# Performance work log

Hardware: AMD Instinct MI355X
Metric: run time of the kernel (lower is better)

The kernel has to match this reference:

```python
import jax, jax.numpy as jnp
import numpy as np

EMBED_DIM = 1024
NUM_HEADS = 16
HEAD_DIM = EMBED_DIM // NUM_HEADS
BATCH = 8
SEQ = 1024


def setup_inputs() -> dict:
    key = jax.random.key(0)
    ks = jax.random.split(key, 10)
    s = 1.0 / np.sqrt(EMBED_DIM)
    x = jax.random.normal(ks[0], (BATCH, SEQ, EMBED_DIM), dtype=jnp.float32)
    mask = jax.random.randint(ks[1], (BATCH, SEQ), 0, 2, dtype=jnp.int32)
    mk = lambda k: (jax.random.normal(k, (EMBED_DIM, EMBED_DIM), dtype=jnp.float32) * s)
    return {
        "x": x, "mask": mask,
        "Wq": mk(ks[2]), "bq": jnp.zeros((EMBED_DIM,), jnp.float32),
        "Wk": mk(ks[3]), "bk": jnp.zeros((EMBED_DIM,), jnp.float32),
        "Wv": mk(ks[4]), "bv": jnp.zeros((EMBED_DIM,), jnp.float32),
        "Wo": mk(ks[5]), "bo": jnp.zeros((EMBED_DIM,), jnp.float32),
    }


def _split_heads(t):
    # (B, S, E) -> (B, H, S, D)
    B, S, _ = t.shape
    return t.reshape(B, S, NUM_HEADS, HEAD_DIM).transpose(0, 2, 1, 3)


def reference(x, mask, Wq, bq, Wk, bk, Wv, bv, Wo, bo):
    B, S, E = x.shape
    # torch Linear: y = x @ W.T + b, weight shape (out, in)
    Q = _split_heads(jnp.einsum('bse,oe->bso', x, Wq) + bq)
    K = _split_heads(jnp.einsum('bse,oe->bso', x, Wk) + bk)
    V = _split_heads(jnp.einsum('bse,oe->bso', x, Wv) + bv)
    scores = jnp.einsum('bhqd,bhkd->bhqk', Q, K) / np.sqrt(HEAD_DIM)
    scores = jnp.clip(scores, -50.0, 50.0)
    m = (mask == 0)[:, None, None, :]  # (B,1,1,S)
    scores = jnp.where(m, jnp.float32(-1e9), scores)
    scores = jnp.where(jnp.isfinite(scores), scores, jnp.zeros_like(scores))
    aw = jax.nn.softmax(scores, axis=-1)
    aw = jnp.where(jnp.isfinite(aw), aw, jnp.zeros_like(aw))
    aw = aw / (aw.sum(axis=-1, keepdims=True) + 1e-10)
    # dropout is identity in eval mode
    attended = jnp.einsum('bhqk,bhkd->bhqd', aw, V)
    attended = attended.transpose(0, 2, 1, 3).reshape(B, S, E)
    output = jnp.einsum('bse,oe->bso', attended, Wo) + bo
    return (output, aw)
```

## Files before the change

### kernel.cpp

```cpp
#include <hip/hip_runtime.h>

typedef _Float16 f16x8 __attribute__((ext_vector_type(8)));
typedef float    f32x4 __attribute__((ext_vector_type(4)));

#define SEQL 1024
#define EMB  1024
#define NH   16
#define HD   64
#define BATCH 8

__global__ __launch_bounds__(256) void k_cvt_f32_f16(const float* __restrict__ in,
                                                     _Float16* __restrict__ out,
                                                     int n8) {
  int i = blockIdx.x * 256 + threadIdx.x;
  if (i >= n8) return;
  const float4* p = (const float4*)in;
  float4 a = p[2 * i], b = p[2 * i + 1];
  f16x8 o;
  o[0] = (_Float16)a.x; o[1] = (_Float16)a.y; o[2] = (_Float16)a.z; o[3] = (_Float16)a.w;
  o[4] = (_Float16)b.x; o[5] = (_Float16)b.y; o[6] = (_Float16)b.z; o[7] = (_Float16)b.w;
  ((f16x8*)out)[i] = o;
}

template <int OUT_F16>
__global__ __launch_bounds__(256) void k_gemm_nt(const _Float16* __restrict__ A,
                                                 const _Float16* __restrict__ B,
                                                 const float* __restrict__ bias,
                                                 void* __restrict__ Cv,
                                                 int M, int N, int K) {
  __shared__ __align__(16) _Float16 As[128 * 32];
  __shared__ __align__(16) _Float16 Bs[128 * 32];
  const int nb = N >> 7;
  const int bm = (int)blockIdx.x / nb, bn = (int)blockIdx.x % nb;
  const int m0 = bm << 7, n0 = bn << 7;
  const int tid = threadIdx.x;
  const int wave = tid >> 6, lane = tid & 63, quad = lane >> 4, l16 = lane & 15;
  const int wm = (wave & 1) << 6, wn = (wave >> 1) << 6;

  f32x4 acc[4][4] = {};

  const int c0 = tid, c1 = tid + 256;
  const int row0 = c0 >> 2, ko0 = (c0 & 3) << 3;
  const int row1 = c1 >> 2, ko1 = (c1 & 3) << 3;

  for (int k0 = 0; k0 < K; k0 += 32) {
    __syncthreads();
    ((uint4*)As)[c0] = *(const uint4*)(A + (size_t)(m0 + row0) * K + k0 + ko0);
    ((uint4*)As)[c1] = *(const uint4*)(A + (size_t)(m0 + row1) * K + k0 + ko1);
    ((uint4*)Bs)[c0] = *(const uint4*)(B + (size_t)(n0 + row0) * K + k0 + ko0);
    ((uint4*)Bs)[c1] = *(const uint4*)(B + (size_t)(n0 + row1) * K + k0 + ko1);
    __syncthreads();

    f16x8 af[4], bf[4];
#pragma unroll
    for (int i = 0; i < 4; ++i)
      af[i] = *(const f16x8*)(As + ((wm + (i << 4) + l16) << 5) + (quad << 3));
#pragma unroll
    for (int i = 0; i < 4; ++i)
      bf[i] = *(const f16x8*)(Bs + ((wn + (i << 4) + l16) << 5) + (quad << 3));
#pragma unroll
    for (int i = 0; i < 4; ++i)
#pragma unroll
      for (int j = 0; j < 4; ++j)
        acc[i][j] = __builtin_amdgcn_mfma_f32_16x16x32_f16(af[i], bf[j], acc[i][j], 0, 0, 0);
  }

#pragma unroll
  for (int j = 0; j < 4; ++j) {
    int col = n0 + wn + (j << 4) + l16;
    float bb = bias[col];
#pragma unroll
    for (int i = 0; i < 4; ++i) {
      int rowb = m0 + wm + (i << 4) + (quad << 2);
#pragma unroll
      for (int r = 0; r < 4; ++r) {
        float v = acc[i][j][r] + bb;
        if (OUT_F16)
          ((_Float16*)Cv)[(size_t)(rowb + r) * N + col] = (_Float16)v;
        else
          ((float*)Cv)[(size_t)(rowb + r) * N + col] = v;
      }
    }
  }
}

__global__ __launch_bounds__(256) void k_transpose_v(const _Float16* __restrict__ V,
                                                     _Float16* __restrict__ Vt) {
  int tid = blockIdx.x * 256 + threadIdx.x;
  int d = tid & 63;
  int s0 = ((tid >> 6) & 127) << 3;
  int h = (tid >> 13) & 15;
  int b = tid >> 17;
  const _Float16* src = V + ((size_t)(b * SEQL + s0)) * EMB + h * HD + d;
  f16x8 t;
#pragma unroll
  for (int j = 0; j < 8; ++j) t[j] = src[(size_t)j * EMB];
  *(f16x8*)(Vt + ((size_t)((b * NH + h) * HD + d)) * SEQL + s0) = t;
}

__global__ __launch_bounds__(256) void k_scores_softmax(const _Float16* __restrict__ Q,
                                                        const _Float16* __restrict__ Kmat,
                                                        const int* __restrict__ mask,
                                                        float* __restrict__ aw) {
  const int qt = blockIdx.x, h = blockIdx.y, b = blockIdx.z;
  const int tid = threadIdx.x;
  const int wave = tid >> 6, lane = tid & 63, quad = lane >> 4, l16 = lane & 15;

  const _Float16* Qbase = Q + ((size_t)(b * SEQL + qt * 16 + l16)) * EMB + h * HD + quad * 8;
  f16x8 qf0 = *(const f16x8*)(Qbase);
  f16x8 qf1 = *(const f16x8*)(Qbase + 32);

  float p[16][4];
  float mr[4], lr[4];
#pragma unroll
  for (int r = 0; r < 4; ++r) mr[r] = -3.0e38f;

  const int* mrow = mask + b * SEQL;

#pragma unroll
  for (int ct = 0; ct < 16; ++ct) {
    int col = wave * 256 + ct * 16 + l16;
    const _Float16* Kb = Kmat + ((size_t)(b * SEQL + col)) * EMB + h * HD + quad * 8;
    f16x8 kf0 = *(const f16x8*)(Kb);
    f16x8 kf1 = *(const f16x8*)(Kb + 32);
    f32x4 acc = {};
    acc = __builtin_amdgcn_mfma_f32_16x16x32_f16(qf0, kf0, acc, 0, 0, 0);
    acc = __builtin_amdgcn_mfma_f32_16x16x32_f16(qf1, kf1, acc, 0, 0, 0);
    bool mk = (mrow[col] == 0);
#pragma unroll
    for (int r = 0; r < 4; ++r) {
      float s = acc[r] * 0.125f;
      s = fminf(fmaxf(s, -50.f), 50.f);
      if (mk) s = -1.0e9f;
      p[ct][r] = s;
      mr[r] = fmaxf(mr[r], s);
    }
  }

#pragma unroll
  for (int r = 0; r < 4; ++r) {
    float m = mr[r];
    m = fmaxf(m, __shfl_xor(m, 1, 16));
    m = fmaxf(m, __shfl_xor(m, 2, 16));
    m = fmaxf(m, __shfl_xor(m, 4, 16));
    m = fmaxf(m, __shfl_xor(m, 8, 16));
    mr[r] = m;
  }

#pragma unroll
  for (int r = 0; r < 4; ++r) lr[r] = 0.f;
#pragma unroll
  for (int ct = 0; ct < 16; ++ct) {
#pragma unroll
    for (int r = 0; r < 4; ++r) {
      float e = __expf(p[ct][r] - mr[r]);
      p[ct][r] = e;
      lr[r] += e;
    }
  }
#pragma unroll
  for (int r = 0; r < 4; ++r) {
    float l = lr[r];
    l += __shfl_xor(l, 1, 16);
    l += __shfl_xor(l, 2, 16);
    l += __shfl_xor(l, 4, 16);
    l += __shfl_xor(l, 8, 16);
    lr[r] = l;
  }

  __shared__ float sm[4][16], sl[4][16];
  if (l16 == 0) {
#pragma unroll
    for (int r = 0; r < 4; ++r) {
      sm[wave][quad * 4 + r] = mr[r];
      sl[wave][quad * 4 + r] = lr[r];
    }
  }
  __syncthreads();

  float f[4];
#pragma unroll
  for (int r = 0; r < 4; ++r) {
    int row = quad * 4 + r;
    float M = fmaxf(fmaxf(sm[0][row], sm[1][row]), fmaxf(sm[2][row], sm[3][row]));
    float L = sl[0][row] * __expf(sm[0][row] - M) + sl[1][row] * __expf(sm[1][row] - M) +
              sl[2][row] * __expf(sm[2][row] - M) + sl[3][row] * __expf(sm[3][row] - M);
    f[r] = __expf(mr[r] - M) / L;
  }

  float* awb = aw + (((size_t)(b * NH + h)) * SEQL + qt * 16) * SEQL;
#pragma unroll
  for (int ct = 0; ct < 16; ++ct) {
    int col = wave * 256 + ct * 16 + l16;
#pragma unroll
    for (int r = 0; r < 4; ++r) {
      awb[(size_t)(quad * 4 + r) * SEQL + col] = p[ct][r] * f[r];
    }
  }
}

__global__ __launch_bounds__(256) void k_attn_pv(const float* __restrict__ aw,
                                                 const _Float16* __restrict__ Vt,
                                                 _Float16* __restrict__ att) {
  const int mt = blockIdx.x;
  const int h = blockIdx.y, b = blockIdx.z;
  const int tid = threadIdx.x;
  const int wave = tid >> 6, lane = tid & 63, quad = lane >> 4, l16 = lane & 15;
  const int m0 = mt * 64 + wave * 16;

  const float* awrow = aw + (((size_t)(b * NH + h)) * SEQL + m0 + l16) * SEQL;
  const _Float16* vtb = Vt + ((size_t)(b * NH + h)) * HD * SEQL;

  f32x4 acc[4] = {};

  for (int k0 = 0; k0 < SEQL; k0 += 32) {
    float4 a0 = *(const float4*)(awrow + k0 + quad * 8);
    float4 a1 = *(const float4*)(awrow + k0 + quad * 8 + 4);
    f16x8 af;
    af[0] = (_Float16)a0.x; af[1] = (_Float16)a0.y; af[2] = (_Float16)a0.z; af[3] = (_Float16)a0.w;
    af[4] = (_Float16)a1.x; af[5] = (_Float16)a1.y; af[6] = (_Float16)a1.z; af[7] = (_Float16)a1.w;
#pragma unroll
    for (int nt = 0; nt < 4; ++nt) {
      f16x8 bf = *(const f16x8*)(vtb + (size_t)(nt * 16 + l16) * SEQL + k0 + quad * 8);
      acc[nt] = __builtin_amdgcn_mfma_f32_16x16x32_f16(af, bf, acc[nt], 0, 0, 0);
    }
  }

#pragma unroll
  for (int nt = 0; nt < 4; ++nt) {
    int d = nt * 16 + l16;
#pragma unroll
    for (int r = 0; r < 4; ++r) {
      int srow = m0 + quad * 4 + r;
      att[((size_t)(b * SEQL + srow)) * EMB + h * HD + d] = (_Float16)acc[nt][r];
    }
  }
}

extern "C" void kernel_launch(void* const* d_in, const int* in_sizes, int n_in,
                              void* d_out, int out_size, void* d_ws, size_t ws_size,
                              hipStream_t stream) {
  const float* x  = (const float*)d_in[0];
  const int* mask = (const int*)d_in[1];
  const float* Wq = (const float*)d_in[2];
  const float* bq = (const float*)d_in[3];
  const float* Wk = (const float*)d_in[4];
  const float* bk = (const float*)d_in[5];
  const float* Wv = (const float*)d_in[6];
  const float* bv = (const float*)d_in[7];
  const float* Wo = (const float*)d_in[8];
  const float* bo = (const float*)d_in[9];

  float* out = (float*)d_out;
  float* aw = out + (size_t)BATCH * SEQL * EMB;

  char* ws = (char*)d_ws;
  _Float16* x16  = (_Float16*)(ws);
  _Float16* Wq16 = (_Float16*)(ws + ((size_t)16 << 20));
  _Float16* Wk16 = (_Float16*)(ws + ((size_t)18 << 20));
  _Float16* Wv16 = (_Float16*)(ws + ((size_t)20 << 20));
  _Float16* Wo16 = (_Float16*)(ws + ((size_t)22 << 20));
  _Float16* Q16  = (_Float16*)(ws + ((size_t)24 << 20));
  _Float16* K16  = (_Float16*)(ws + ((size_t)40 << 20));
  _Float16* V16  = (_Float16*)(ws + ((size_t)56 << 20));
  _Float16* Vt16  = x16;
  _Float16* att16 = Q16;

  const int M = BATCH * SEQL, N = EMB, K = EMB;

  k_cvt_f32_f16<<<4096, 256, 0, stream>>>(x, x16, (M * EMB) / 8);
  k_cvt_f32_f16<<<512, 256, 0, stream>>>(Wq, Wq16, (EMB * EMB) / 8);
  k_cvt_f32_f16<<<512, 256, 0, stream>>>(Wk, Wk16, (EMB * EMB) / 8);
  k_cvt_f32_f16<<<512, 256, 0, stream>>>(Wv, Wv16, (EMB * EMB) / 8);
  k_cvt_f32_f16<<<512, 256, 0, stream>>>(Wo, Wo16, (EMB * EMB) / 8);

  k_gemm_nt<1><<<(M / 128) * (N / 128), 256, 0, stream>>>(x16, Wq16, bq, Q16, M, N, K);
  k_gemm_nt<1><<<(M / 128) * (N / 128), 256, 0, stream>>>(x16, Wk16, bk, K16, M, N, K);
  k_gemm_nt<1><<<(M / 128) * (N / 128), 256, 0, stream>>>(x16, Wv16, bv, V16, M, N, K);

  k_transpose_v<<<4096, 256, 0, stream>>>(V16, Vt16);

  k_scores_softmax<<<dim3(SEQL / 16, NH, BATCH), 256, 0, stream>>>(Q16, K16, mask, aw);

  k_attn_pv<<<dim3(SEQL / 64, NH, BATCH), 256, 0, stream>>>(aw, Vt16, att16);

  k_gemm_nt<0><<<(M / 128) * (N / 128), 256, 0, stream>>>(att16, Wo16, bo, out, M, N, K);
}
```

Before: 1.044 ms.

## Fuse QKV GEMMs, merge conversions, fuse softmax with PV, use direct-to-LDS loads

```diff
diff --git a/kernel.cpp b/kernel.cpp
--- a/kernel.cpp
+++ b/kernel.cpp
@@ -1,4 +1,5 @@
 #include <hip/hip_runtime.h>
+#include <stdint.h>
 
 typedef _Float16 f16x8 __attribute__((ext_vector_type(8)));
 typedef float    f32x4 __attribute__((ext_vector_type(4)));
@@ -8,18 +9,52 @@
 #define NH   16
 #define HD   64
 #define BATCH 8
-
-__global__ __launch_bounds__(256) void k_cvt_f32_f16(const float* __restrict__ in,
-                                                     _Float16* __restrict__ out,
-                                                     int n8) {
-  int i = blockIdx.x * 256 + threadIdx.x;
-  if (i >= n8) return;
+#define QKVN 3072
+
+__device__ __forceinline__ void gll16(const void* g, void* l) {
+  __builtin_amdgcn_global_load_lds(
+      (const __attribute__((address_space(1))) unsigned int*)(uintptr_t)g,
+      (__attribute__((address_space(3))) unsigned int*)(uintptr_t)l, 16, 0, 0);
+}
+
+__device__ __forceinline__ void cvt8(const float* __restrict__ in,
+                                     _Float16* __restrict__ out, int i) {
   const float4* p = (const float4*)in;
   float4 a = p[2 * i], b = p[2 * i + 1];
   f16x8 o;
   o[0] = (_Float16)a.x; o[1] = (_Float16)a.y; o[2] = (_Float16)a.z; o[3] = (_Float16)a.w;
   o[4] = (_Float16)b.x; o[5] = (_Float16)b.y; o[6] = (_Float16)b.z; o[7] = (_Float16)b.w;
   ((f16x8*)out)[i] = o;
+}
+
+__global__ __launch_bounds__(256) void k_prep(const float* __restrict__ x,
+                                              const float* __restrict__ Wq,
+                                              const float* __restrict__ Wk,
+                                              const float* __restrict__ Wv,
+                                              const float* __restrict__ Wo,
+                                              const float* __restrict__ bq,
+                                              const float* __restrict__ bk,
+                                              const float* __restrict__ bv,
+                                              _Float16* __restrict__ x16,
+                                              _Float16* __restrict__ Wqkv16,
+                                              _Float16* __restrict__ Wo16,
+                                              float* __restrict__ bqkv) {
+  const int bid = blockIdx.x, tid = threadIdx.x;
+  if (bid < 4096) {
+    cvt8(x, x16, bid * 256 + tid);
+  } else if (bid < 4608) {
+    cvt8(Wq, Wqkv16, (bid - 4096) * 256 + tid);
+  } else if (bid < 5120) {
+    cvt8(Wk, Wqkv16 + (size_t)EMB * EMB, (bid - 4608) * 256 + tid);
+  } else if (bid < 5632) {
+    cvt8(Wv, Wqkv16 + (size_t)2 * EMB * EMB, (bid - 5120) * 256 + tid);
+  } else if (bid < 6144) {
+    cvt8(Wo, Wo16, (bid - 5632) * 256 + tid);
+  } else {
+    int i = (bid - 6144) * 256 + tid;
+    float v = (i < 1024) ? bq[i] : (i < 2048 ? bk[i - 1024] : bv[i - 2048]);
+    bqkv[i] = v;
+  }
 }
 
 template <int OUT_F16>
@@ -42,13 +77,17 @@
   const int c0 = tid, c1 = tid + 256;
   const int row0 = c0 >> 2, ko0 = (c0 & 3) << 3;
   const int row1 = c1 >> 2, ko1 = (c1 & 3) << 3;
+  const _Float16* a0 = A + (size_t)(m0 + row0) * K + ko0;
+  const _Float16* a1 = A + (size_t)(m0 + row1) * K + ko1;
+  const _Float16* b0 = B + (size_t)(n0 + row0) * K + ko0;
+  const _Float16* b1 = B + (size_t)(n0 + row1) * K + ko1;
 
   for (int k0 = 0; k0 < K; k0 += 32) {
     __syncthreads();
-    ((uint4*)As)[c0] = *(const uint4*)(A + (size_t)(m0 + row0) * K + k0 + ko0);
-    ((uint4*)As)[c1] = *(const uint4*)(A + (size_t)(m0 + row1) * K + k0 + ko1);
-    ((uint4*)Bs)[c0] = *(const uint4*)(B + (size_t)(n0 + row0) * K + k0 + ko0);
-    ((uint4*)Bs)[c1] = *(const uint4*)(B + (size_t)(n0 + row1) * K + k0 + ko1);
+    gll16(a0 + k0, As + (size_t)c0 * 8);
+    gll16(a1 + k0, As + (size_t)c1 * 8);
+    gll16(b0 + k0, Bs + (size_t)c0 * 8);
+    gll16(b1 + k0, Bs + (size_t)c1 * 8);
     __syncthreads();
 
     f16x8 af[4], bf[4];
@@ -84,29 +123,38 @@
   }
 }
 
-__global__ __launch_bounds__(256) void k_transpose_v(const _Float16* __restrict__ V,
+__global__ __launch_bounds__(256) void k_transpose_v(const _Float16* __restrict__ QKV,
                                                      _Float16* __restrict__ Vt) {
   int tid = blockIdx.x * 256 + threadIdx.x;
   int d = tid & 63;
   int s0 = ((tid >> 6) & 127) << 3;
   int h = (tid >> 13) & 15;
   int b = tid >> 17;
-  const _Float16* src = V + ((size_t)(b * SEQL + s0)) * EMB + h * HD + d;
+  const _Float16* src = QKV + ((size_t)(b * SEQL + s0)) * QKVN + 2048 + h * HD + d;
   f16x8 t;
 #pragma unroll
-  for (int j = 0; j < 8; ++j) t[j] = src[(size_t)j * EMB];
+  for (int j = 0; j < 8; ++j) t[j] = src[(size_t)j * QKVN];
   *(f16x8*)(Vt + ((size_t)((b * NH + h) * HD + d)) * SEQL + s0) = t;
 }
 
-__global__ __launch_bounds__(256) void k_scores_softmax(const _Float16* __restrict__ Q,
-                                                        const _Float16* __restrict__ Kmat,
-                                                        const int* __restrict__ mask,
-                                                        float* __restrict__ aw) {
+#define PPAD 272
+#define OPAD 68
+
+__global__ __launch_bounds__(256) void k_attn_fused(const _Float16* __restrict__ QKV,
+                                                    const _Float16* __restrict__ Vt,
+                                                    const int* __restrict__ mask,
+                                                    float* __restrict__ aw,
+                                                    _Float16* __restrict__ att) {
+  __shared__ __align__(16) _Float16 pbuf[4][16 * PPAD];
+  __shared__ float obuf[4][16 * OPAD];
+  __shared__ float sm[4][16], sl[4][16];
+
   const int qt = blockIdx.x, h = blockIdx.y, b = blockIdx.z;
   const int tid = threadIdx.x;
   const int wave = tid >> 6, lane = tid & 63, quad = lane >> 4, l16 = lane & 15;
 
-  const _Float16* Qbase = Q + ((size_t)(b * SEQL + qt * 16 + l16)) * EMB + h * HD + quad * 8;
+  const _Float16* Qbase =
+      QKV + ((size_t)(b * SEQL + qt * 16 + l16)) * QKVN + h * HD + quad * 8;
   f16x8 qf0 = *(const f16x8*)(Qbase);
   f16x8 qf1 = *(const f16x8*)(Qbase + 32);
 
@@ -116,11 +164,12 @@
   for (int r = 0; r < 4; ++r) mr[r] = -3.0e38f;
 
   const int* mrow = mask + b * SEQL;
+  const _Float16* Kb0 = QKV + (size_t)b * SEQL * QKVN + 1024 + h * HD + quad * 8;
 
 #pragma unroll
   for (int ct = 0; ct < 16; ++ct) {
     int col = wave * 256 + ct * 16 + l16;
-    const _Float16* Kb = Kmat + ((size_t)(b * SEQL + col)) * EMB + h * HD + quad * 8;
+    const _Float16* Kb = Kb0 + (size_t)col * QKVN;
     f16x8 kf0 = *(const f16x8*)(Kb);
     f16x8 kf1 = *(const f16x8*)(Kb + 32);
     f32x4 acc = {};
@@ -146,7 +195,6 @@
     m = fmaxf(m, __shfl_xor(m, 8, 16));
     mr[r] = m;
   }
-
 #pragma unroll
   for (int r = 0; r < 4; ++r) lr[r] = 0.f;
 #pragma unroll
@@ -167,8 +215,6 @@
     l += __shfl_xor(l, 8, 16);
     lr[r] = l;
   }
-
-  __shared__ float sm[4][16], sl[4][16];
   if (l16 == 0) {
 #pragma unroll
     for (int r = 0; r < 4; ++r) {
@@ -189,50 +235,46 @@
   }
 
   float* awb = aw + (((size_t)(b * NH + h)) * SEQL + qt * 16) * SEQL;
+  _Float16* pw = pbuf[wave];
 #pragma unroll
   for (int ct = 0; ct < 16; ++ct) {
-    int col = wave * 256 + ct * 16 + l16;
 #pragma unroll
     for (int r = 0; r < 4; ++r) {
-      awb[(size_t)(quad * 4 + r) * SEQL + col] = p[ct][r] * f[r];
-    }
-  }
-}
-
-__global__ __launch_bounds__(256) void k_attn_pv(const float* __restrict__ aw,
-                                                 const _Float16* __restrict__ Vt,
-                                                 _Float16* __restrict__ att) {
-  const int mt = blockIdx.x;
-  const int h = blockIdx.y, b = blockIdx.z;
-  const int tid = threadIdx.x;
-  const int wave = tid >> 6, lane = tid & 63, quad = lane >> 4, l16 = lane & 15;
-  const int m0 = mt * 64 + wave * 16;
-
-  const float* awrow = aw + (((size_t)(b * NH + h)) * SEQL + m0 + l16) * SEQL;
-  const _Float16* vtb = Vt + ((size_t)(b * NH + h)) * HD * SEQL;
-
-  f32x4 acc[4] = {};
-
-  for (int k0 = 0; k0 < SEQL; k0 += 32) {
-    float4 a0 = *(const float4*)(awrow + k0 + quad * 8);
-    float4 a1 = *(const float4*)(awrow + k0 + quad * 8 + 4);
-    f16x8 af;
-    af[0] = (_Float16)a0.x; af[1] = (_Float16)a0.y; af[2] = (_Float16)a0.z; af[3] = (_Float16)a0.w;
-    af[4] = (_Float16)a1.x; af[5] = (_Float16)a1.y; af[6] = (_Float16)a1.z; af[7] = (_Float16)a1.w;
+      float v = p[ct][r] * f[r];
+      awb[(size_t)(quad * 4 + r) * SEQL + wave * 256 + ct * 16 + l16] = v;
+      pw[(quad * 4 + r) * PPAD + ct * 16 + l16] = (_Float16)v;
+    }
+  }
+
+  f32x4 opv[4] = {};
+  const _Float16* vtb =
+      Vt + ((size_t)(b * NH + h)) * HD * SEQL + wave * 256 + quad * 8;
+#pragma unroll
+  for (int k = 0; k < 256; k += 32) {
+    f16x8 af = *(const f16x8*)(pw + l16 * PPAD + k + quad * 8);
 #pragma unroll
     for (int nt = 0; nt < 4; ++nt) {
-      f16x8 bf = *(const f16x8*)(vtb + (size_t)(nt * 16 + l16) * SEQL + k0 + quad * 8);
-      acc[nt] = __builtin_amdgcn_mfma_f32_16x16x32_f16(af, bf, acc[nt], 0, 0, 0);
-    }
-  }
-
-#pragma unroll
-  for (int nt = 0; nt < 4; ++nt) {
-    int d = nt * 16 + l16;
-#pragma unroll
-    for (int r = 0; r < 4; ++r) {
-      int srow = m0 + quad * 4 + r;
-      att[((size_t)(b * SEQL + srow)) * EMB + h * HD + d] = (_Float16)acc[nt][r];
+      f16x8 bf = *(const f16x8*)(vtb + (size_t)(nt * 16 + l16) * SEQL + k);
+      opv[nt] = __builtin_amdgcn_mfma_f32_16x16x32_f16(af, bf, opv[nt], 0, 0, 0);
+    }
+  }
+
+#pragma unroll
+  for (int nt = 0; nt < 4; ++nt)
+#pragma unroll
+    for (int r = 0; r < 4; ++r)
+      obuf[wave][(quad * 4 + r) * OPAD + nt * 16 + l16] = opv[nt][r];
+  __syncthreads();
+
+  {
+    int col = tid & 63;
+    int r0 = tid >> 6;
+#pragma unroll
+    for (int i = 0; i < 4; ++i) {
+      int row = r0 + i * 4;
+      float o = obuf[0][row * OPAD + col] + obuf[1][row * OPAD + col] +
+                obuf[2][row * OPAD + col] + obuf[3][row * OPAD + col];
+      att[((size_t)(b * SEQL + qt * 16 + row)) * EMB + h * HD + col] = (_Float16)o;
     }
   }
 }
@@ -255,34 +297,26 @@
   float* aw = out + (size_t)BATCH * SEQL * EMB;
 
   char* ws = (char*)d_ws;
-  _Float16* x16  = (_Float16*)(ws);
-  _Float16* Wq16 = (_Float16*)(ws + ((size_t)16 << 20));
-  _Float16* Wk16 = (_Float16*)(ws + ((size_t)18 << 20));
-  _Float16* Wv16 = (_Float16*)(ws + ((size_t)20 << 20));
-  _Float16* Wo16 = (_Float16*)(ws + ((size_t)22 << 20));
-  _Float16* Q16  = (_Float16*)(ws + ((size_t)24 << 20));
-  _Float16* K16  = (_Float16*)(ws + ((size_t)40 << 20));
-  _Float16* V16  = (_Float16*)(ws + ((size_t)56 << 20));
-  _Float16* Vt16  = x16;
-  _Float16* att16 = Q16;
-
-  const int M = BATCH * SEQL, N = EMB, K = EMB;
-
-  k_cvt_f32_f16<<<4096, 256, 0, stream>>>(x, x16, (M * EMB) / 8);
-  k_cvt_f32_f16<<<512, 256, 0, stream>>>(Wq, Wq16, (EMB * EMB) / 8);
-  k_cvt_f32_f16<<<512, 256, 0, stream>>>(Wk, Wk16, (EMB * EMB) / 8);
-  k_cvt_f32_f16<<<512, 256, 0, stream>>>(Wv, Wv16, (EMB * EMB) / 8);
-  k_cvt_f32_f16<<<512, 256, 0, stream>>>(Wo, Wo16, (EMB * EMB) / 8);
-
-  k_gemm_nt<1><<<(M / 128) * (N / 128), 256, 0, stream>>>(x16, Wq16, bq, Q16, M, N, K);
-  k_gemm_nt<1><<<(M / 128) * (N / 128), 256, 0, stream>>>(x16, Wk16, bk, K16, M, N, K);
-  k_gemm_nt<1><<<(M / 128) * (N / 128), 256, 0, stream>>>(x16, Wv16, bv, V16, M, N, K);
-
-  k_transpose_v<<<4096, 256, 0, stream>>>(V16, Vt16);
-
-  k_scores_softmax<<<dim3(SEQL / 16, NH, BATCH), 256, 0, stream>>>(Q16, K16, mask, aw);
-
-  k_attn_pv<<<dim3(SEQL / 64, NH, BATCH), 256, 0, stream>>>(aw, Vt16, att16);
-
-  k_gemm_nt<0><<<(M / 128) * (N / 128), 256, 0, stream>>>(att16, Wo16, bo, out, M, N, K);
-}
+  _Float16* x16    = (_Float16*)(ws);
+  _Float16* Wqkv16 = (_Float16*)(ws + ((size_t)16 << 20));
+  _Float16* Wo16   = (_Float16*)(ws + ((size_t)22 << 20));
+  float*    bqkv   = (float*)   (ws + ((size_t)24 << 20));
+  _Float16* QKV16  = (_Float16*)(ws + ((size_t)25 << 20));
+  _Float16* Vt16   = (_Float16*)(ws + ((size_t)73 << 20));
+  _Float16* att16  = (_Float16*)(ws + ((size_t)89 << 20));
+
+  const int M = BATCH * SEQL;
+
+  k_prep<<<6156, 256, 0, stream>>>(x, Wq, Wk, Wv, Wo, bq, bk, bv,
+                                   x16, Wqkv16, Wo16, bqkv);
+
+  k_gemm_nt<1><<<(M / 128) * (QKVN / 128), 256, 0, stream>>>(x16, Wqkv16, bqkv, QKV16,
+                                                             M, QKVN, EMB);
+
+  k_transpose_v<<<4096, 256, 0, stream>>>(QKV16, Vt16);
+
+  k_attn_fused<<<dim3(SEQL / 16, NH, BATCH), 256, 0, stream>>>(QKV16, Vt16, mask, aw, att16);
+
+  k_gemm_nt<0><<<(M / 128) * (EMB / 128), 256, 0, stream>>>(att16, Wo16, bo, out,
+                                                            M, EMB, EMB);
+}
```

Result: faster. 914.5 us (-12.4%).
